# Optimization experiments

Hardware: AMD Instinct MI355X
Metric: run time of the kernel (lower is better)

## Reference

```python
import jax, jax.numpy as jnp
import numpy as np

D_MODEL = 1024
NUM_HEADS = 16
D_K = D_MODEL // NUM_HEADS
SCALE = D_K ** -0.5
NEG = -1e9


def setup_inputs() -> dict:
    key = jax.random.key(0)
    ks = jax.random.split(key, 10)
    B, S = 4, 2048
    x = jax.random.normal(ks[0], (B, S, D_MODEL), dtype=jnp.float32)
    # causal mask: True = masked position (upper triangle)
    mask = jnp.broadcast_to(jnp.triu(jnp.ones((S, S), dtype=bool), k=1), (B, S, S))
    init = 1.0 / np.sqrt(D_MODEL)
    def lin(kw, kb):
        W = jax.random.uniform(kw, (D_MODEL, D_MODEL), jnp.float32, -init, init)
        b = jax.random.uniform(kb, (D_MODEL,), jnp.float32, -init, init)
        return W, b
    Wq, bq = lin(ks[1], ks[2])
    Wk, bk = lin(ks[3], ks[4])
    Wv, bv = lin(ks[5], ks[6])
    Wo, bo = lin(ks[7], ks[8])
    return {"x": x, "mask": mask, "Wq": Wq, "bq": bq, "Wk": Wk, "bk": bk,
            "Wv": Wv, "bv": bv, "Wo": Wo, "bo": bo}


def reference(x, mask, Wq, bq, Wk, bk, Wv, bv, Wo, bo):
    B, S, _ = x.shape
    # projections; weights stored as [in, out] (torch Linear applies x @ W.T; here W already transposed)
    def split_heads(t):
        return t.reshape(B, S, NUM_HEADS, D_K).transpose(0, 2, 1, 3)  # [B,H,S,d_k]
    q = split_heads(x @ Wq + bq)
    k = split_heads(x @ Wk + bk)
    v = split_heads(x @ Wv + bv)
    scores = jnp.einsum('bhqd,bhkd->bhqk', q, k) * SCALE  # [B,H,S,S]
    scores = jnp.where(mask[:, None, :, :], NEG, scores)
    attn = jax.nn.softmax(scores, axis=-1)
    # dropout is identity in eval mode
    out = jnp.einsum('bhqk,bhkd->bhqd', attn, v)
    out = out.transpose(0, 2, 1, 3).reshape(B, S, D_MODEL)
    return out @ Wo + bo
```

## Files before the change

kernel.cpp:

```cpp
#include <hip/hip_runtime.h>
#include <hip/hip_bf16.h>

#define D_MODEL 1024
#define NUM_HEADS 16
#define D_K 64
#define S_LEN 2048
#define BATCH 4

typedef unsigned short u16;
typedef __attribute__((ext_vector_type(8))) short bf16x8;
typedef __attribute__((ext_vector_type(4))) float f32x4;

#define MFMA16 __builtin_amdgcn_mfma_f32_16x16x32_bf16

#define Q_SCALE 0.18033688011112042f

__device__ __forceinline__ float bf2f(u16 u) {
    union { unsigned int i; float f; } v; v.i = ((unsigned int)u) << 16; return v.f;
}
__device__ __forceinline__ u16 f2bf(float f) {
    union { unsigned int i; float f; } v; v.f = f;
    unsigned int x = v.i;
    return (u16)((x + 0x7FFFu + ((x >> 16) & 1u)) >> 16);
}
__device__ __forceinline__ unsigned int cvtpk(float lo, float hi) {
    unsigned int r;
    asm("v_cvt_pk_bf16_f32 %0, %1, %2" : "=v"(r) : "v"(lo), "v"(hi));
    return r;
}

__device__ __forceinline__ void gload16(const u16* g, u16* l) {
    __builtin_amdgcn_global_load_lds(
        (const __attribute__((address_space(1))) unsigned int*)g,
        (__attribute__((address_space(3))) unsigned int*)l, 16, 0, 0);
}

__global__ __launch_bounds__(256) void convert_x(
    const float* __restrict__ x, u16* __restrict__ xb)
{
    const size_t i = ((size_t)blockIdx.x * 256 + threadIdx.x) * 8;
    float4 a = *reinterpret_cast<const float4*>(x + i);
    float4 b = *reinterpret_cast<const float4*>(x + i + 4);
    bf16x8 o;
    o[0] = (short)f2bf(a.x); o[1] = (short)f2bf(a.y);
    o[2] = (short)f2bf(a.z); o[3] = (short)f2bf(a.w);
    o[4] = (short)f2bf(b.x); o[5] = (short)f2bf(b.y);
    o[6] = (short)f2bf(b.z); o[7] = (short)f2bf(b.w);
    *reinterpret_cast<bf16x8*>(xb + i) = o;
}

__global__ __launch_bounds__(256) void transpose_w(
    const float* __restrict__ W0, const float* __restrict__ W1,
    const float* __restrict__ W2, const float* __restrict__ W3,
    u16* __restrict__ T0, u16* __restrict__ T1,
    u16* __restrict__ T2, u16* __restrict__ T3)
{
    const float* W; u16* T;
    switch (blockIdx.z & 3) {
        case 0:  W = W0; T = T0; break;
        case 1:  W = W1; T = T1; break;
        case 2:  W = W2; T = T2; break;
        default: W = W3; T = T3; break;
    }
    __shared__ u16 S[64][72];
    const int tid = threadIdx.x;
    const int k0 = blockIdx.y * 64, n0 = blockIdx.x * 64;

    const int k = tid >> 2, nb = (tid & 3) * 16;
    #pragma unroll
    for (int c = 0; c < 4; ++c) {
        float4 v = *reinterpret_cast<const float4*>(
            W + (size_t)(k0 + k) * D_MODEL + n0 + nb + c * 4);
        S[nb + c * 4 + 0][k] = f2bf(v.x);
        S[nb + c * 4 + 1][k] = f2bf(v.y);
        S[nb + c * 4 + 2][k] = f2bf(v.z);
        S[nb + c * 4 + 3][k] = f2bf(v.w);
    }
    __syncthreads();
    const int n = tid >> 2, kb = (tid & 3) * 16;
    #pragma unroll
    for (int c = 0; c < 2; ++c) {
        bf16x8 o;
        #pragma unroll
        for (int e = 0; e < 8; ++e) o[e] = (short)S[n][kb + c * 8 + e];
        *reinterpret_cast<bf16x8*>(T + (size_t)(n0 + n) * D_MODEL + k0 + kb + c * 8) = o;
    }
}

template <typename TC>
__device__ __forceinline__ void gemm_body(
    const u16* __restrict__ A, const u16* __restrict__ BT,
    const float* __restrict__ bias, TC* __restrict__ C,
    u16* Al, u16* Bl, float oscale)
{
    const int tid = threadIdx.x;
    const int w = tid >> 6, lane = tid & 63;
    const int g = lane >> 4, c16 = lane & 15;
    const int wr = w >> 1, wc = w & 1;
    const int m0 = blockIdx.y * 128, n0 = blockIdx.x * 128;

    int rS[4], uS[4];
    #pragma unroll
    for (int i = 0; i < 4; ++i) {
        const int p = i * 256 + tid;
        rS[i] = p >> 3;
        uS[i] = ((p & 7) ^ (rS[i] & 7)) * 8;
    }

    f32x4 acc[4][4];
    #pragma unroll
    for (int mi = 0; mi < 4; ++mi)
        #pragma unroll
        for (int ni = 0; ni < 4; ++ni) acc[mi][ni] = (f32x4){0.f, 0.f, 0.f, 0.f};

    for (int k0 = 0; k0 < D_MODEL; k0 += 64) {
        #pragma unroll
        for (int i = 0; i < 4; ++i) {
            gload16(A + (size_t)(m0 + rS[i]) * D_MODEL + k0 + uS[i],
                    Al + (size_t)(i * 256 + w * 64) * 8);
            gload16(BT + (size_t)(n0 + rS[i]) * D_MODEL + k0 + uS[i],
                    Bl + (size_t)(i * 256 + w * 64) * 8);
        }
        __syncthreads();

        #pragma unroll
        for (int s = 0; s < 2; ++s) {
            bf16x8 af[4], bfr[4];
            #pragma unroll
            for (int mi = 0; mi < 4; ++mi) {
                const int r = wr * 64 + mi * 16 + c16;
                af[mi] = *reinterpret_cast<const bf16x8*>(
                    &Al[((r << 3) + ((s * 4 + g) ^ (r & 7))) * 8]);
            }
            #pragma unroll
            for (int ni = 0; ni < 4; ++ni) {
                const int r = wc * 64 + ni * 16 + c16;
                bfr[ni] = *reinterpret_cast<const bf16x8*>(
                    &Bl[((r << 3) + ((s * 4 + g) ^ (r & 7))) * 8]);
            }
            #pragma unroll
            for (int mi = 0; mi < 4; ++mi)
                #pragma unroll
                for (int ni = 0; ni < 4; ++ni)
                    acc[mi][ni] = MFMA16(af[mi], bfr[ni], acc[mi][ni], 0, 0, 0);
        }
        __syncthreads();
    }

    float bc[4];
    #pragma unroll
    for (int ni = 0; ni < 4; ++ni) bc[ni] = bias[n0 + wc * 64 + ni * 16 + c16];

    #pragma unroll
    for (int mi = 0; mi < 4; ++mi) {
        #pragma unroll
        for (int ni = 0; ni < 4; ++ni) {
            const int col = n0 + wc * 64 + ni * 16 + c16;
            #pragma unroll
            for (int r = 0; r < 4; ++r) {
                const int row = m0 + wr * 64 + mi * 16 + g * 4 + r;
                const float v = (acc[mi][ni][r] + bc[ni]) * oscale;
                if constexpr (sizeof(TC) == 4) {
                    C[(size_t)row * D_MODEL + col] = v;
                } else {
                    C[(size_t)row * D_MODEL + col] = f2bf(v);
                }
            }
        }
    }
}

__global__ __launch_bounds__(256) void gemm_qkv(
    const u16* __restrict__ A,
    const u16* __restrict__ BTq, const u16* __restrict__ BTk, const u16* __restrict__ BTv,
    const float* __restrict__ bq, const float* __restrict__ bk, const float* __restrict__ bv,
    u16* __restrict__ Cq, u16* __restrict__ Ck, u16* __restrict__ Cv)
{
    __shared__ u16 Al[128 * 64];
    __shared__ u16 Bl[128 * 64];
    const u16* BT; const float* bias; u16* C; float sc;
    switch (blockIdx.z) {
        case 0:  BT = BTq; bias = bq; C = Cq; sc = Q_SCALE; break;
        case 1:  BT = BTk; bias = bk; C = Ck; sc = 1.f; break;
        default: BT = BTv; bias = bv; C = Cv; sc = 1.f; break;
    }
    gemm_body<u16>(A, BT, bias, C, Al, Bl, sc);
}

__global__ __launch_bounds__(256) void gemm_out(
    const u16* __restrict__ A, const u16* __restrict__ BT,
    const float* __restrict__ bias, float* __restrict__ C)
{
    __shared__ u16 Al[128 * 64];
    __shared__ u16 Bl[128 * 64];
    gemm_body<float>(A, BT, bias, C, Al, Bl, 1.f);
}

__global__ __launch_bounds__(256) void transpose_v(
    const u16* __restrict__ Vb, u16* __restrict__ VT)
{
    __shared__ u16 T[64 * 65];
    const int i  = blockIdx.x;
    const int bh = i >> 5, jt = i & 31;
    const int b  = bh >> 4, h = bh & 15;
    const int j0 = jt * 64, hd = h * 64;
    const int tid = threadIdx.x;

    #pragma unroll
    for (int it = 0; it < 2; ++it) {
        int seg = it * 256 + tid;
        int jr = seg >> 3, d0 = (seg & 7) * 8;
        bf16x8 v = *reinterpret_cast<const bf16x8*>(
            Vb + ((size_t)(b * S_LEN + j0 + jr)) * D_MODEL + hd + d0);
        #pragma unroll
        for (int e = 0; e < 8; ++e) T[jr * 65 + d0 + e] = (u16)v[e];
    }
    __syncthreads();
    #pragma unroll
    for (int it = 0; it < 2; ++it) {
        int seg = it * 256 + tid;
        int d = seg >> 3, uj = (seg & 7) * 8;
        bf16x8 o;
        #pragma unroll
        for (int e = 0; e < 8; ++e) o[e] = (short)T[(uj + e) * 65 + d];
        *reinterpret_cast<bf16x8*>(
            VT + ((size_t)bh * 64 + d) * S_LEN + j0 + uj) = o;
    }
}

__global__ __launch_bounds__(512, 4) void flash_attn(
    const u16* __restrict__ Qb, const u16* __restrict__ Kb,
    const u16* __restrict__ VT, u16* __restrict__ AO)
{
    __shared__ u16 K_lds[64 * 64];
    __shared__ u16 V_lds[64 * 64];
    __shared__ u16 P_lds[8 * 16 * 64];

    const int i  = blockIdx.x;
    const int bh = (i & 7) * 8 + ((i >> 3) & 7);
    const int p  = i >> 6;
    const int b  = bh >> 4, h = bh & 15, hd = h * 64;

    const int tid = threadIdx.x;
    const int w = tid >> 6, lane = tid & 63;
    const int wq = w & 3;
    const int g = lane >> 4, c16 = lane & 15;

    const int qt = (w < 4) ? p : (31 - p);
    const int q0 = qt * 64 + wq * 16;

    const size_t kbase  = (size_t)b * S_LEN * D_MODEL + hd;
    const size_t vtbase = (size_t)bh * 64 * S_LEN;
    u16* Pw = &P_lds[w * 1024];

    const f32x4 ZERO = {0.f, 0.f, 0.f, 0.f};
    const f32x4 NEGI = {-1e30f, -1e30f, -1e30f, -1e30f};

    const int rK = tid >> 3;
    const int uK = ((tid & 7) ^ (rK & 7)) * 8;

    const size_t qrow = ((size_t)b * S_LEN + q0 + c16) * D_MODEL + hd;
    const bf16x8 qf0 = *reinterpret_cast<const bf16x8*>(Qb + qrow + g * 8);
    const bf16x8 qf1 = *reinterpret_cast<const bf16x8*>(Qb + qrow + 32 + g * 8);

    f32x4 acc[4];
    #pragma unroll
    for (int dt = 0; dt < 4; ++dt) acc[dt] = ZERO;
    float m = -1e30f, lp = 0.f;

    const int nt = 32 - p;
    for (int jt = 0; jt < nt; ++jt) {
        const int j0 = jt * 64;

        __syncthreads();
        gload16(Kb + kbase + (size_t)(j0 + rK) * D_MODEL + uK, K_lds + (size_t)tid * 8);
        gload16(VT + vtbase + (size_t)rK * S_LEN + j0 + uK,    V_lds + (size_t)tid * 8);
        __syncthreads();

        if (jt > qt) continue;
        const bool dtile = (jt == qt);

        f32x4 st[4];
        #pragma unroll
        for (int kt = 0; kt < 4; ++kt) {
            if (dtile && kt > wq) { st[kt] = NEGI; continue; }
            const int row = kt * 16 + c16;
            const bf16x8 kf0 = *reinterpret_cast<const bf16x8*>(
                &K_lds[row * 64 + ((g ^ (row & 7)) << 3)]);
            const bf16x8 kf1 = *reinterpret_cast<const bf16x8*>(
                &K_lds[row * 64 + (((4 + g) ^ (row & 7)) << 3)]);
            f32x4 t = MFMA16(kf0, qf0, ZERO, 0, 0, 0);
            t = MFMA16(kf1, qf1, t, 0, 0, 0);
            if (dtile && kt == wq) {
                #pragma unroll
                for (int r = 0; r < 4; ++r)
                    if (g * 4 + r > c16) t[r] = -1e30f;
            }
            st[kt] = t;
        }

        float mx = st[0][0];
        #pragma unroll
        for (int kt = 0; kt < 4; ++kt)
            #pragma unroll
            for (int r = 0; r < 4; ++r) mx = fmaxf(mx, st[kt][r]);
        mx = fmaxf(mx, __shfl_xor(mx, 16));
        mx = fmaxf(mx, __shfl_xor(mx, 32));

        if (__any(mx > m + 11.5f)) {
            const float mn = fmaxf(m, mx);
            const float co = __builtin_amdgcn_exp2f(m - mn);
            lp *= co;
            m = mn;
            float cor[4];
            #pragma unroll
            for (int r = 0; r < 4; ++r) cor[r] = __shfl(co, g * 4 + r);
            #pragma unroll
            for (int dt = 0; dt < 4; ++dt)
                #pragma unroll
                for (int r = 0; r < 4; ++r) acc[dt][r] *= cor[r];
        }

        float tsum = 0.f;
        #pragma unroll
        for (int kt = 0; kt < 4; ++kt) {
            const float p0 = __builtin_amdgcn_exp2f(st[kt][0] - m);
            const float p1 = __builtin_amdgcn_exp2f(st[kt][1] - m);
            const float p2 = __builtin_amdgcn_exp2f(st[kt][2] - m);
            const float p3 = __builtin_amdgcn_exp2f(st[kt][3] - m);
            tsum += (p0 + p1) + (p2 + p3);
            uint2 pw;
            pw.x = cvtpk(p0, p1);
            pw.y = cvtpk(p2, p3);
            const int u = kt * 2 + (g >> 1);
            *reinterpret_cast<uint2*>(
                &Pw[c16 * 64 + ((u ^ (c16 & 7)) << 3) + (g & 1) * 4]) = pw;
        }
        lp += tsum;

        #pragma unroll
        for (int c32 = 0; c32 < 2; ++c32) {
            if (dtile && c32 == 1 && wq < 2) continue;
            const bf16x8 pf = *reinterpret_cast<const bf16x8*>(
                &Pw[c16 * 64 + (((c32 * 4 + g) ^ (c16 & 7)) << 3)]);
            #pragma unroll
            for (int dt = 0; dt < 4; ++dt) {
                const int vrow = dt * 16 + c16;
                const bf16x8 vf = *reinterpret_cast<const bf16x8*>(
                    &V_lds[vrow * 64 + (((c32 * 4 + g) ^ (vrow & 7)) << 3)]);
                acc[dt] = MFMA16(pf, vf, acc[dt], 0, 0, 0);
            }
        }
    }

    float lt = lp + __shfl_xor(lp, 16);
    lt += __shfl_xor(lt, 32);
    const float inv = 1.f / lt;
    float invr[4];
    #pragma unroll
    for (int r = 0; r < 4; ++r) invr[r] = __shfl(inv, g * 4 + r);

    #pragma unroll
    for (int dt = 0; dt < 4; ++dt) {
        #pragma unroll
        for (int r = 0; r < 4; ++r) {
            const size_t orow =
                ((size_t)b * S_LEN + q0 + g * 4 + r) * D_MODEL + hd + dt * 16 + c16;
            AO[orow] = f2bf(acc[dt][r] * invr[r]);
        }
    }
}

extern "C" void kernel_launch(void* const* d_in, const int* in_sizes, int n_in,
                              void* d_out, int out_size, void* d_ws, size_t ws_size,
                              hipStream_t stream) {
    const float* x  = (const float*)d_in[0];
    const float* Wq = (const float*)d_in[2];
    const float* bq = (const float*)d_in[3];
    const float* Wk = (const float*)d_in[4];
    const float* bk = (const float*)d_in[5];
    const float* Wv = (const float*)d_in[6];
    const float* bv = (const float*)d_in[7];
    const float* Wo = (const float*)d_in[8];
    const float* bo = (const float*)d_in[9];
    float* out = (float*)d_out;

    const int M = BATCH * S_LEN;
    const size_t tsz = (size_t)M * D_MODEL;
    const size_t wsz = (size_t)D_MODEL * D_MODEL;

    u16* xb  = (u16*)d_ws;
    u16* Qb  = xb + tsz;
    u16* Kb  = Qb + tsz;
    u16* Vb  = Kb + tsz;
    u16* VT  = Vb + tsz;
    u16* WTq = VT + tsz;
    u16* WTk = WTq + wsz;
    u16* WTv = WTk + wsz;
    u16* WTo = WTv + wsz;
    u16* AO  = Vb;

    convert_x<<<(int)(tsz / (256 * 8)), 256, 0, stream>>>(x, xb);
    transpose_w<<<dim3(16, 16, 4), 256, 0, stream>>>(
        Wq, Wk, Wv, Wo, WTq, WTk, WTv, WTo);

    gemm_qkv<<<dim3(8, 64, 3), 256, 0, stream>>>(
        xb, WTq, WTk, WTv, bq, bk, bv, Qb, Kb, Vb);

    transpose_v<<<2048, 256, 0, stream>>>(Vb, VT);
    flash_attn<<<1024, 512, 0, stream>>>(Qb, Kb, VT, AO);

    gemm_out<<<dim3(8, 64), 256, 0, stream>>>(AO, WTo, bo, out);
}
```

Before: 200.5 us.

## Read K and V fragments straight from global memory in flash attention, one q-tile per block

The flash attention kernel no longer stages K and V tiles through LDS with block-wide barriers. Each wave loads its K and V MFMA fragments directly from global memory (relying on L1/L2 reuse). Blocks shrink to 4 waves covering a single query tile, replacing the paired p/31-p scheme, and the grid doubles to 2048 blocks with heaviest tiles scheduled first. Sched barriers pin instruction ordering. This removes the syncthreads and the LDS round trip, at the cost of redundant global/cache traffic across waves and uncoalesced 16-byte row loads.

```diff
diff --git a/kernel.cpp b/kernel.cpp
--- a/kernel.cpp
+++ b/kernel.cpp
@@ -228,26 +228,21 @@
     }
 }
 
-__global__ __launch_bounds__(512, 4) void flash_attn(
+__global__ __launch_bounds__(256, 4) void flash_attn(
     const u16* __restrict__ Qb, const u16* __restrict__ Kb,
     const u16* __restrict__ VT, u16* __restrict__ AO)
 {
-    __shared__ u16 K_lds[64 * 64];
-    __shared__ u16 V_lds[64 * 64];
-    __shared__ u16 P_lds[8 * 16 * 64];
+    __shared__ u16 P_lds[4 * 16 * 64];
 
     const int i  = blockIdx.x;
     const int bh = (i & 7) * 8 + ((i >> 3) & 7);
-    const int p  = i >> 6;
+    const int qt = 31 - (i >> 6);
     const int b  = bh >> 4, h = bh & 15, hd = h * 64;
 
     const int tid = threadIdx.x;
     const int w = tid >> 6, lane = tid & 63;
-    const int wq = w & 3;
     const int g = lane >> 4, c16 = lane & 15;
-
-    const int qt = (w < 4) ? p : (31 - p);
-    const int q0 = qt * 64 + wq * 16;
+    const int q0 = qt * 64 + w * 16;
 
     const size_t kbase  = (size_t)b * S_LEN * D_MODEL + hd;
     const size_t vtbase = (size_t)bh * 64 * S_LEN;
@@ -256,9 +251,6 @@
     const f32x4 ZERO = {0.f, 0.f, 0.f, 0.f};
     const f32x4 NEGI = {-1e30f, -1e30f, -1e30f, -1e30f};
 
-    const int rK = tid >> 3;
-    const int uK = ((tid & 7) ^ (rK & 7)) * 8;
-
     const size_t qrow = ((size_t)b * S_LEN + q0 + c16) * D_MODEL + hd;
     const bf16x8 qf0 = *reinterpret_cast<const bf16x8*>(Qb + qrow + g * 8);
     const bf16x8 qf1 = *reinterpret_cast<const bf16x8*>(Qb + qrow + 32 + g * 8);
@@ -268,30 +260,26 @@
     for (int dt = 0; dt < 4; ++dt) acc[dt] = ZERO;
     float m = -1e30f, lp = 0.f;
 
-    const int nt = 32 - p;
-    for (int jt = 0; jt < nt; ++jt) {
+    for (int jt = 0; jt <= qt; ++jt) {
         const int j0 = jt * 64;
-
-        __syncthreads();
-        gload16(Kb + kbase + (size_t)(j0 + rK) * D_MODEL + uK, K_lds + (size_t)tid * 8);
-        gload16(VT + vtbase + (size_t)rK * S_LEN + j0 + uK,    V_lds + (size_t)tid * 8);
-        __syncthreads();
-
-        if (jt > qt) continue;
         const bool dtile = (jt == qt);
 
+        bf16x8 kf0[4], kf1[4];
+        #pragma unroll
+        for (int kt = 0; kt < 4; ++kt) {
+            if (dtile && kt > w) continue;
+            const u16* kp = Kb + kbase + (size_t)(j0 + kt * 16 + c16) * D_MODEL + g * 8;
+            kf0[kt] = *reinterpret_cast<const bf16x8*>(kp);
+            kf1[kt] = *reinterpret_cast<const bf16x8*>(kp + 32);
+        }
+
         f32x4 st[4];
         #pragma unroll
         for (int kt = 0; kt < 4; ++kt) {
-            if (dtile && kt > wq) { st[kt] = NEGI; continue; }
-            const int row = kt * 16 + c16;
-            const bf16x8 kf0 = *reinterpret_cast<const bf16x8*>(
-                &K_lds[row * 64 + ((g ^ (row & 7)) << 3)]);
-            const bf16x8 kf1 = *reinterpret_cast<const bf16x8*>(
-                &K_lds[row * 64 + (((4 + g) ^ (row & 7)) << 3)]);
-            f32x4 t = MFMA16(kf0, qf0, ZERO, 0, 0, 0);
-            t = MFMA16(kf1, qf1, t, 0, 0, 0);
-            if (dtile && kt == wq) {
+            if (dtile && kt > w) { st[kt] = NEGI; continue; }
+            f32x4 t = MFMA16(kf0[kt], qf0, ZERO, 0, 0, 0);
+            t = MFMA16(kf1[kt], qf1, t, 0, 0, 0);
+            if (dtile && kt == w) {
                 #pragma unroll
                 for (int r = 0; r < 4; ++r)
                     if (g * 4 + r > c16) t[r] = -1e30f;
@@ -338,19 +326,22 @@
         }
         lp += tsum;
 
+        __builtin_amdgcn_sched_barrier(0x7F);
+
         #pragma unroll
         for (int c32 = 0; c32 < 2; ++c32) {
-            if (dtile && c32 == 1 && wq < 2) continue;
+            if (dtile && c32 == 1 && w < 2) continue;
             const bf16x8 pf = *reinterpret_cast<const bf16x8*>(
                 &Pw[c16 * 64 + (((c32 * 4 + g) ^ (c16 & 7)) << 3)]);
             #pragma unroll
             for (int dt = 0; dt < 4; ++dt) {
-                const int vrow = dt * 16 + c16;
                 const bf16x8 vf = *reinterpret_cast<const bf16x8*>(
-                    &V_lds[vrow * 64 + (((c32 * 4 + g) ^ (vrow & 7)) << 3)]);
+                    VT + vtbase + (size_t)(dt * 16 + c16) * S_LEN + j0 + c32 * 32 + g * 8);
                 acc[dt] = MFMA16(pf, vf, acc[dt], 0, 0, 0);
             }
         }
+
+        __builtin_amdgcn_sched_barrier(0x7F);
     }
 
     float lt = lp + __shfl_xor(lp, 16);
@@ -408,7 +399,7 @@
         xb, WTq, WTk, WTv, bq, bk, bv, Qb, Kb, Vb);
 
     transpose_v<<<2048, 256, 0, stream>>>(Vb, VT);
-    flash_attn<<<1024, 512, 0, stream>>>(Qb, Kb, VT, AO);
+    flash_attn<<<2048, 256, 0, stream>>>(Qb, Kb, VT, AO);
 
     gemm_out<<<dim3(8, 64), 256, 0, stream>>>(AO, WTo, bo, out);
 }
```

After: 350.3 us. +74.7%, slower.

## Double-buffer K/V tiles in flash attention and prefetch next tile

Applied to the files above, without the earlier changes.

Turns the single K/V LDS buffer into two buffers and issues the global-to-LDS load for the next key tile before computing on the current one. This removes one barrier per iteration and hides load latency behind the MFMA and softmax work. It also raises the launch-bounds occupancy hint from 4 to 6, and adds s_setprio around the MFMA sections plus sched_barriers. In exchange the kernel uses 16 KB more LDS per block, which may cap occupancy and conflicts with the higher occupancy hint.

```diff
diff --git a/kernel.cpp b/kernel.cpp
--- a/kernel.cpp
+++ b/kernel.cpp
@@ -228,13 +228,13 @@
     }
 }
 
-__global__ __launch_bounds__(512, 4) void flash_attn(
+__global__ __launch_bounds__(512, 6) void flash_attn(
     const u16* __restrict__ Qb, const u16* __restrict__ Kb,
     const u16* __restrict__ VT, u16* __restrict__ AO)
 {
-    __shared__ u16 K_lds[64 * 64];
-    __shared__ u16 V_lds[64 * 64];
-    __shared__ u16 P_lds[8 * 16 * 64];
+    __shared__ u16 K_lds[2][4096];
+    __shared__ u16 V_lds[2][4096];
+    __shared__ u16 P_lds[8 * 1024];
 
     const int i  = blockIdx.x;
     const int bh = (i & 7) * 8 + ((i >> 3) & 7);
@@ -269,88 +269,107 @@
     float m = -1e30f, lp = 0.f;
 
     const int nt = 32 - p;
+
+    gload16(Kb + kbase + (size_t)rK * D_MODEL + uK, &K_lds[0][tid * 8]);
+    gload16(VT + vtbase + (size_t)rK * S_LEN + uK,  &V_lds[0][tid * 8]);
+    __syncthreads();
+
+    int cur = 0;
     for (int jt = 0; jt < nt; ++jt) {
-        const int j0 = jt * 64;
+        if (jt + 1 < nt) {
+            const int j0n = (jt + 1) * 64;
+            gload16(Kb + kbase + (size_t)(j0n + rK) * D_MODEL + uK, &K_lds[cur ^ 1][tid * 8]);
+            gload16(VT + vtbase + (size_t)rK * S_LEN + j0n + uK,    &V_lds[cur ^ 1][tid * 8]);
+        }
+
+        if (jt <= qt) {
+            const bool dtile = (jt == qt);
+            const u16* kl = K_lds[cur];
+            const u16* vl = V_lds[cur];
+
+            f32x4 st[4];
+            __builtin_amdgcn_s_setprio(1);
+            #pragma unroll
+            for (int kt = 0; kt < 4; ++kt) {
+                if (dtile && kt > wq) { st[kt] = NEGI; continue; }
+                const int row = kt * 16 + c16;
+                const bf16x8 kf0 = *reinterpret_cast<const bf16x8*>(
+                    &kl[row * 64 + ((g ^ (row & 7)) << 3)]);
+                const bf16x8 kf1 = *reinterpret_cast<const bf16x8*>(
+                    &kl[row * 64 + (((4 + g) ^ (row & 7)) << 3)]);
+                f32x4 t = MFMA16(kf0, qf0, ZERO, 0, 0, 0);
+                t = MFMA16(kf1, qf1, t, 0, 0, 0);
+                if (dtile && kt == wq) {
+                    #pragma unroll
+                    for (int r = 0; r < 4; ++r)
+                        if (g * 4 + r > c16) t[r] = -1e30f;
+                }
+                st[kt] = t;
+            }
+            __builtin_amdgcn_s_setprio(0);
+
+            float mx = st[0][0];
+            #pragma unroll
+            for (int kt = 0; kt < 4; ++kt)
+                #pragma unroll
+                for (int r = 0; r < 4; ++r) mx = fmaxf(mx, st[kt][r]);
+            mx = fmaxf(mx, __shfl_xor(mx, 16));
+            mx = fmaxf(mx, __shfl_xor(mx, 32));
+
+            if (__any(mx > m + 11.5f)) {
+                const float mn = fmaxf(m, mx);
+                const float co = __builtin_amdgcn_exp2f(m - mn);
+                lp *= co;
+                m = mn;
+                float cor[4];
+                #pragma unroll
+                for (int r = 0; r < 4; ++r) cor[r] = __shfl(co, g * 4 + r);
+                #pragma unroll
+                for (int dt = 0; dt < 4; ++dt)
+                    #pragma unroll
+                    for (int r = 0; r < 4; ++r) acc[dt][r] *= cor[r];
+            }
+
+            float tsum = 0.f;
+            #pragma unroll
+            for (int kt = 0; kt < 4; ++kt) {
+                const float p0 = __builtin_amdgcn_exp2f(st[kt][0] - m);
+                const float p1 = __builtin_amdgcn_exp2f(st[kt][1] - m);
+                const float p2 = __builtin_amdgcn_exp2f(st[kt][2] - m);
+                const float p3 = __builtin_amdgcn_exp2f(st[kt][3] - m);
+                tsum += (p0 + p1) + (p2 + p3);
+                uint2 pw;
+                pw.x = cvtpk(p0, p1);
+                pw.y = cvtpk(p2, p3);
+                const int u = kt * 2 + (g >> 1);
+                *reinterpret_cast<uint2*>(
+                    &Pw[c16 * 64 + ((u ^ (c16 & 7)) << 3) + (g & 1) * 4]) = pw;
+            }
+            lp += tsum;
+
+            __builtin_amdgcn_sched_barrier(0x7F);
+
+            __builtin_amdgcn_s_setprio(1);
+            #pragma unroll
+            for (int c32 = 0; c32 < 2; ++c32) {
+                if (dtile && c32 == 1 && wq < 2) continue;
+                const bf16x8 pf = *reinterpret_cast<const bf16x8*>(
+                    &Pw[c16 * 64 + (((c32 * 4 + g) ^ (c16 & 7)) << 3)]);
+                #pragma unroll
+                for (int dt = 0; dt < 4; ++dt) {
+                    const int vrow = dt * 16 + c16;
+                    const bf16x8 vf = *reinterpret_cast<const bf16x8*>(
+                        &vl[vrow * 64 + (((c32 * 4 + g) ^ (vrow & 7)) << 3)]);
+                    acc[dt] = MFMA16(pf, vf, acc[dt], 0, 0, 0);
+                }
+            }
+            __builtin_amdgcn_s_setprio(0);
+
+            __builtin_amdgcn_sched_barrier(0x7F);
+        }
 
         __syncthreads();
-        gload16(Kb + kbase + (size_t)(j0 + rK) * D_MODEL + uK, K_lds + (size_t)tid * 8);
-        gload16(VT + vtbase + (size_t)rK * S_LEN + j0 + uK,    V_lds + (size_t)tid * 8);
-        __syncthreads();
-
-        if (jt > qt) continue;
-        const bool dtile = (jt == qt);
-
-        f32x4 st[4];
-        #pragma unroll
-        for (int kt = 0; kt < 4; ++kt) {
-            if (dtile && kt > wq) { st[kt] = NEGI; continue; }
-            const int row = kt * 16 + c16;
-            const bf16x8 kf0 = *reinterpret_cast<const bf16x8*>(
-                &K_lds[row * 64 + ((g ^ (row & 7)) << 3)]);
-            const bf16x8 kf1 = *reinterpret_cast<const bf16x8*>(
-                &K_lds[row * 64 + (((4 + g) ^ (row & 7)) << 3)]);
-            f32x4 t = MFMA16(kf0, qf0, ZERO, 0, 0, 0);
-            t = MFMA16(kf1, qf1, t, 0, 0, 0);
-            if (dtile && kt == wq) {
-                #pragma unroll
-                for (int r = 0; r < 4; ++r)
-                    if (g * 4 + r > c16) t[r] = -1e30f;
-            }
-            st[kt] = t;
-        }
-
-        float mx = st[0][0];
-        #pragma unroll
-        for (int kt = 0; kt < 4; ++kt)
-            #pragma unroll
-            for (int r = 0; r < 4; ++r) mx = fmaxf(mx, st[kt][r]);
-        mx = fmaxf(mx, __shfl_xor(mx, 16));
-        mx = fmaxf(mx, __shfl_xor(mx, 32));
-
-        if (__any(mx > m + 11.5f)) {
-            const float mn = fmaxf(m, mx);
-            const float co = __builtin_amdgcn_exp2f(m - mn);
-            lp *= co;
-            m = mn;
-            float cor[4];
-            #pragma unroll
-            for (int r = 0; r < 4; ++r) cor[r] = __shfl(co, g * 4 + r);
-            #pragma unroll
-            for (int dt = 0; dt < 4; ++dt)
-                #pragma unroll
-                for (int r = 0; r < 4; ++r) acc[dt][r] *= cor[r];
-        }
-
-        float tsum = 0.f;
-        #pragma unroll
-        for (int kt = 0; kt < 4; ++kt) {
-            const float p0 = __builtin_amdgcn_exp2f(st[kt][0] - m);
-            const float p1 = __builtin_amdgcn_exp2f(st[kt][1] - m);
-            const float p2 = __builtin_amdgcn_exp2f(st[kt][2] - m);
-            const float p3 = __builtin_amdgcn_exp2f(st[kt][3] - m);
-            tsum += (p0 + p1) + (p2 + p3);
-            uint2 pw;
-            pw.x = cvtpk(p0, p1);
-            pw.y = cvtpk(p2, p3);
-            const int u = kt * 2 + (g >> 1);
-            *reinterpret_cast<uint2*>(
-                &Pw[c16 * 64 + ((u ^ (c16 & 7)) << 3) + (g & 1) * 4]) = pw;
-        }
-        lp += tsum;
-
-        #pragma unroll
-        for (int c32 = 0; c32 < 2; ++c32) {
-            if (dtile && c32 == 1 && wq < 2) continue;
-            const bf16x8 pf = *reinterpret_cast<const bf16x8*>(
-                &Pw[c16 * 64 + (((c32 * 4 + g) ^ (c16 & 7)) << 3)]);
-            #pragma unroll
-            for (int dt = 0; dt < 4; ++dt) {
-                const int vrow = dt * 16 + c16;
-                const bf16x8 vf = *reinterpret_cast<const bf16x8*>(
-                    &V_lds[vrow * 64 + (((c32 * 4 + g) ^ (vrow & 7)) << 3)]);
-                acc[dt] = MFMA16(pf, vf, acc[dt], 0, 0, 0);
-            }
-        }
+        cur ^= 1;
     }
 
     float lt = lp + __shfl_xor(lp, 16);
```

Result: no change. 202.1 us (+0.8%).
